# Optimization experiments

Hardware: AMD Instinct MI355X
Metric: run time of the kernel (lower is better)

## Reference

```python
import jax, jax.numpy as jnp
import numpy as np

STATE_DIM = 128
ACT_DIM = 32
ENC_K = 10   # encoder_spine_dim
DEC_K = 10   # decoder_dim
H0, H1 = 2048, 2048
BATCH = 16384
MAX_ACTION = 1.0
STD0 = 0.3872983346207417  # sqrt(0.15)


def setup_inputs() -> dict:
    key = jax.random.key(0)
    ks = jax.random.split(key, 10)
    state = jax.random.normal(ks[0], (BATCH, STATE_DIM), dtype=jnp.float32)
    # encoder params: mean linspace over mean_range, std constant
    mean_enc = jnp.broadcast_to(jnp.linspace(-3.0, 3.0, ENC_K, dtype=jnp.float32),
                                (1, STATE_DIM, ENC_K))
    std_enc = jnp.full((1, STATE_DIM, ENC_K), STD0, dtype=jnp.float32)
    def lin(k, fan_in, fan_out):
        bound = 1.0 / np.sqrt(fan_in)
        k1, k2 = jax.random.split(k)
        W = jax.random.uniform(k1, (fan_out, fan_in), jnp.float32, -bound, bound)
        b = jax.random.uniform(k2, (fan_out,), jnp.float32, -bound, bound)
        return W, b
    W1, b1 = lin(ks[1], STATE_DIM * ENC_K, H0)
    W2, b2 = lin(ks[2], H0, H1)
    W3, b3 = lin(ks[3], H1, ACT_DIM * DEC_K)
    # grouped conv1d: weight [act_dim, 1, dec_k], bias [act_dim]
    bound = 1.0 / np.sqrt(DEC_K)
    Wd = jax.random.uniform(ks[4], (ACT_DIM, 1, DEC_K), jnp.float32, -bound, bound)
    bd = jax.random.uniform(ks[5], (ACT_DIM,), jnp.float32, -bound, bound)
    return {"state": state, "mean_enc": mean_enc, "std_enc": std_enc,
            "W1": W1, "b1": b1, "W2": W2, "b2": b2, "W3": W3, "b3": b3,
            "Wd": Wd, "bd": bd}


def reference(state, mean_enc, std_enc, W1, b1, W2, b2, W3, b3, Wd, bd):
    # Population-coding encoder: sigmoid((obs - mean)/std), flattened
    spine = jax.nn.sigmoid((state[:, :, None] - mean_enc) / std_enc)  # [B, D, K]
    spine = spine.reshape(state.shape[0], -1)                         # [B, D*K]
    a = jax.nn.relu(spine @ W1.T + b1)
    a = jax.nn.relu(a @ W2.T + b2)
    a = a @ W3.T + b3                                                 # [B, A*Kd]
    d = a.reshape(-1, ACT_DIM, DEC_K)                                 # [B, A, Kd]
    # grouped Conv1d with kernel == length => per-channel dot product
    raw = jnp.einsum('bak,ak->ba', d, Wd[:, 0, :]) + bd               # [B, A]
    return MAX_ACTION * jnp.tanh(raw)
```

## Files before the change

### kernel.cpp

```cpp
#include <hip/hip_runtime.h>
#include <hip/hip_bf16.h>
#include <stdint.h>

#define BATCH   16384
#define SDIM    128
#define ENCK    10
#define ADIM    32
#define DECK    10
#define HID     2048
#define KSPINE  1280

typedef __bf16 bf16x8 __attribute__((ext_vector_type(8)));
typedef float  f32x4  __attribute__((ext_vector_type(4)));

typedef __attribute__((address_space(1))) const void kGlobalVoid;
typedef __attribute__((address_space(3))) void       kLdsVoid;

__device__ __forceinline__ unsigned short f2b(float f) {
  union { float f; unsigned u; } v; v.f = f;
  unsigned r = v.u + 0x7fffu + ((v.u >> 16) & 1u);
  return (unsigned short)(r >> 16);
}

__global__ void f2b_kernel(const float* __restrict__ in, unsigned* __restrict__ out, int n2) {
  int i = blockIdx.x * blockDim.x + threadIdx.x;
  if (i >= n2) return;
  float2 v = reinterpret_cast<const float2*>(in)[i];
  out[i] = (unsigned)f2b(v.x) | ((unsigned)f2b(v.y) << 16);
}

__global__ void encoder_kernel(const float* __restrict__ state,
                               const float* __restrict__ mean,
                               const float* __restrict__ stdv,
                               unsigned* __restrict__ spine) {
  int idx = blockIdx.x * blockDim.x + threadIdx.x;
  if (idx >= BATCH * SDIM) return;
  int d = idx & (SDIM - 1);
  float x = state[idx];
  float vals[ENCK];
#pragma unroll
  for (int k = 0; k < ENCK; ++k) {
    float z = (x - mean[d * ENCK + k]) / stdv[d * ENCK + k];
    vals[k] = 1.f / (1.f + __expf(-z));
  }
  unsigned* dst = spine + idx * (ENCK / 2);
#pragma unroll
  for (int k = 0; k < ENCK / 2; ++k)
    dst[k] = (unsigned)f2b(vals[2 * k]) | ((unsigned)f2b(vals[2 * k + 1]) << 16);
}

__global__ void weff_kernel(const float* __restrict__ W3, const float* __restrict__ Wd,
                            unsigned short* __restrict__ Weff) {
  int idx = blockIdx.x * 256 + threadIdx.x;
  int a = idx >> 11, j = idx & 2047;
  float s = 0.f;
#pragma unroll
  for (int k = 0; k < DECK; ++k)
    s += Wd[a * DECK + k] * W3[(size_t)(a * DECK + k) * HID + j];
  Weff[idx] = f2b(s);
}

__global__ void beff_kernel(const float* __restrict__ b3, const float* __restrict__ Wd,
                            const float* __restrict__ bd, float* __restrict__ beff) {
  int a = threadIdx.x;
  if (a >= ADIM) return;
  float s = bd[a];
#pragma unroll
  for (int k = 0; k < DECK; ++k) s += Wd[a * DECK + k] * b3[a * DECK + k];
  beff[a] = s;
}


#define A0B 0
#define B0B 32768
#define A1B 65536
#define B1B 98304

#define FENCE asm volatile("" ::: "memory")

#define STAGE(BASEPTR, R0A, R0B, LDS0, LDS1, KT)                                             \
  __builtin_amdgcn_global_load_lds((kGlobalVoid*)((BASEPTR) + (size_t)((R0A) + rs) * K + (KT) + ce), \
                                   (kLdsVoid*)(smem + (LDS0) + t * 16), 16, 0, 0);           \
  __builtin_amdgcn_global_load_lds((kGlobalVoid*)((BASEPTR) + (size_t)((R0B) + rs) * K + (KT) + ce), \
                                   (kLdsVoid*)(smem + (LDS1) + t * 16), 16, 0, 0);

#define PHASE(mp, ABASE, DOB, BBASE, DOVM, STAGES)                                           \
  do {                                                                                       \
    bf16x8 af[2][2];                                                                         \
    _Pragma("unroll")                                                                        \
    for (int j = 0; j < 2; ++j) {                                                            \
      _Pragma("unroll")                                                                      \
      for (int ks = 0; ks < 2; ++ks) {                                                       \
        int rowl = wr * 128 + ((mp) * 2 + j) * 16 + lr;                                      \
        af[j][ks] = *reinterpret_cast<const bf16x8*>(                                        \
            smem + (ABASE) + rowl * 128 + ((((ks) << 6) | (kh << 4)) ^ swz));                \
      }                                                                                      \
    }                                                                                        \
    if (DOB) {                                                                               \
      _Pragma("unroll")                                                                      \
      for (int n = 0; n < 4; ++n) {                                                          \
        _Pragma("unroll")                                                                    \
        for (int ks = 0; ks < 2; ++ks) {                                                     \
          int rowl = wc * 64 + n * 16 + lr;                                                  \
          bfv[n][ks] = *reinterpret_cast<const bf16x8*>(                                     \
              smem + (BBASE) + rowl * 128 + ((((ks) << 6) | (kh << 4)) ^ swz));              \
        }                                                                                    \
      }                                                                                      \
    }                                                                                        \
    STAGES                                                                                   \
    FENCE;                                                                                   \
    __builtin_amdgcn_s_barrier();                                                            \
    asm volatile("s_waitcnt lgkmcnt(0)" ::: "memory");                                       \
    __builtin_amdgcn_sched_barrier(0);                                                       \
    __builtin_amdgcn_s_setprio(1);                                                           \
    _Pragma("unroll")                                                                        \
    for (int j = 0; j < 2; ++j)                                                              \
      _Pragma("unroll")                                                                      \
      for (int n = 0; n < 4; ++n)                                                            \
        _Pragma("unroll")                                                                    \
        for (int ks = 0; ks < 2; ++ks)                                                       \
          acc[(mp) * 2 + j][n] =                                                             \
              __builtin_amdgcn_mfma_f32_16x16x32_bf16(af[j][ks], bfv[n][ks],                 \
                                                      acc[(mp) * 2 + j][n], 0, 0, 0);        \
    __builtin_amdgcn_s_setprio(0);                                                           \
    if (DOVM) asm volatile("s_waitcnt vmcnt(6)" ::: "memory");                               \
    FENCE;                                                                                   \
    __builtin_amdgcn_s_barrier();                                                            \
  } while (0)

__global__ __launch_bounds__(512, 2) void gemm256(
    const unsigned short* __restrict__ A,
    const unsigned short* __restrict__ Bw,
    const float* __restrict__ bias,
    unsigned short* __restrict__ Cout,
    int K, int NI) {
  __shared__ char smem[131072];

  const int t    = threadIdx.x;
  const int lane = t & 63;
  const int w    = t >> 6;
  const int wr   = w >> 2;
  const int wc   = w & 3;
  const int lr   = lane & 15;
  const int kh   = lane >> 4;
  const int swz  = (lr & 7) << 4;
  const int rs   = t >> 3;
  const int ce   = ((t & 7) ^ (rs & 7)) << 3;

  const int bid = blockIdx.x;
  const int xcd = bid & 7, idx = bid >> 3;
  const int row0 = (xcd * 8 + (idx >> 3)) * 256;
  const int col0 = (idx & 7) * 256;

  f32x4 acc[8][4];
#pragma unroll
  for (int m = 0; m < 8; ++m)
#pragma unroll
    for (int n = 0; n < 4; ++n)
      acc[m][n] = (f32x4){0.f, 0.f, 0.f, 0.f};

  bf16x8 bfv[4][2];

  STAGE(Bw, col0 + 0,   col0 + 64,  B0B + 0,     B0B + 8192,  0);
  STAGE(Bw, col0 + 128, col0 + 192, B0B + 16384, B0B + 24576, 0);
  STAGE(A,  row0 + 0,   row0 + 128, A0B + 0,     A0B + 16384, 0);
  STAGE(A,  row0 + 64,  row0 + 192, A0B + 8192,  A0B + 24576, 0);
  STAGE(Bw, col0 + 0,   col0 + 64,  B1B + 0,     B1B + 8192,  64);
  STAGE(Bw, col0 + 128, col0 + 192, B1B + 16384, B1B + 24576, 64);
  STAGE(A,  row0 + 0,   row0 + 128, A1B + 0,     A1B + 16384, 64);
  asm volatile("s_waitcnt vmcnt(6)" ::: "memory");
  FENCE;
  __builtin_amdgcn_s_barrier();

  for (int i = 0; i < NI; ++i) {
    int kt0 = i << 7;
    int kt1 = kt0 + 64;
    int kt2 = kt0 + 128; if (kt2 >= K) kt2 -= K;
    int kt3 = kt0 + 192; if (kt3 >= K) kt3 -= K;

    PHASE(0, A0B, true,  B0B, false, STAGE(A,  row0 + 64,  row0 + 192, A1B + 8192,  A1B + 24576, kt1));
    PHASE(1, A0B, false, B0B, false, STAGE(Bw, col0 + 0,   col0 + 64,  B0B + 0,     B0B + 8192,  kt2));
    PHASE(2, A0B, false, B0B, false, STAGE(Bw, col0 + 128, col0 + 192, B0B + 16384, B0B + 24576, kt2));
    PHASE(3, A0B, false, B0B, true,  STAGE(A,  row0 + 0,   row0 + 128, A0B + 0,     A0B + 16384, kt2));
    PHASE(0, A1B, true,  B1B, false, STAGE(A,  row0 + 64,  row0 + 192, A0B + 8192,  A0B + 24576, kt2));
    PHASE(1, A1B, false, B1B, false, STAGE(Bw, col0 + 0,   col0 + 64,  B1B + 0,     B1B + 8192,  kt3));
    PHASE(2, A1B, false, B1B, false, STAGE(Bw, col0 + 128, col0 + 192, B1B + 16384, B1B + 24576, kt3));
    PHASE(3, A1B, false, B1B, true,  STAGE(A,  row0 + 0,   row0 + 128, A1B + 0,     A1B + 16384, kt3));
  }

#pragma unroll
  for (int m = 0; m < 8; ++m) {
    int gr0 = row0 + wr * 128 + m * 16 + kh * 4;
#pragma unroll
    for (int n = 0; n < 4; ++n) {
      int gc = col0 + wc * 64 + n * 16 + lr;
      float bv = bias[gc];
#pragma unroll
      for (int v = 0; v < 4; ++v) {
        float val = fmaxf(acc[m][n][v] + bv, 0.f);
        Cout[(size_t)(gr0 + v) * 2048 + gc] = f2b(val);
      }
    }
  }
}

__global__ __launch_bounds__(128) void gemm_skinny(
    const unsigned short* __restrict__ A,
    const unsigned short* __restrict__ Bw,
    const float* __restrict__ beff,
    float* __restrict__ out) {
  const int t = threadIdx.x, lane = t & 63, w = t >> 6;
  const int lr = lane & 15, kh = lane >> 4;
  const int row0 = blockIdx.x * 64 + w * 32;
  f32x4 acc[2][2];
#pragma unroll
  for (int m = 0; m < 2; ++m)
#pragma unroll
    for (int n = 0; n < 2; ++n) acc[m][n] = (f32x4){0.f, 0.f, 0.f, 0.f};

#pragma unroll 4
  for (int kt = 0; kt < HID; kt += 32) {
    bf16x8 af[2], bv[2];
#pragma unroll
    for (int m = 0; m < 2; ++m)
      af[m] = *reinterpret_cast<const bf16x8*>(A + (size_t)(row0 + m * 16 + lr) * HID + kt + kh * 8);
#pragma unroll
    for (int n = 0; n < 2; ++n)
      bv[n] = *reinterpret_cast<const bf16x8*>(Bw + (size_t)(n * 16 + lr) * HID + kt + kh * 8);
#pragma unroll
    for (int m = 0; m < 2; ++m)
#pragma unroll
      for (int n = 0; n < 2; ++n)
        acc[m][n] = __builtin_amdgcn_mfma_f32_16x16x32_bf16(af[m], bv[n], acc[m][n], 0, 0, 0);
  }
#pragma unroll
  for (int m = 0; m < 2; ++m)
#pragma unroll
    for (int n = 0; n < 2; ++n)
#pragma unroll
      for (int v = 0; v < 4; ++v) {
        int row = row0 + m * 16 + kh * 4 + v;
        int col = n * 16 + lr;
        out[(size_t)row * ADIM + col] = tanhf(acc[m][n][v] + beff[col]);
      }
}

extern "C" void kernel_launch(void* const* d_in, const int* in_sizes, int n_in,
                              void* d_out, int out_size, void* d_ws, size_t ws_size,
                              hipStream_t stream) {
  const float* state    = (const float*)d_in[0];
  const float* mean_enc = (const float*)d_in[1];
  const float* std_enc  = (const float*)d_in[2];
  const float* W1 = (const float*)d_in[3];
  const float* b1 = (const float*)d_in[4];
  const float* W2 = (const float*)d_in[5];
  const float* b2 = (const float*)d_in[6];
  const float* W3 = (const float*)d_in[7];
  const float* b3 = (const float*)d_in[8];
  const float* Wd = (const float*)d_in[9];
  const float* bd = (const float*)d_in[10];

  char* ws = (char*)d_ws;
  unsigned short* W1b   = (unsigned short*)(ws + 0);
  unsigned short* W2b   = (unsigned short*)(ws + 5242880);
  unsigned short* Weff  = (unsigned short*)(ws + 13631488);
  float*          beff  = (float*)(ws + 13762560);
  unsigned short* spine = (unsigned short*)(ws + 13762688);
  unsigned short* h1    = (unsigned short*)(ws + 55705728);
  unsigned short* h2    = (unsigned short*)(ws + 122814592);

  f2b_kernel<<<5120, 256, 0, stream>>>(W1, (unsigned*)W1b, 1310720);
  f2b_kernel<<<8192, 256, 0, stream>>>(W2, (unsigned*)W2b, 2097152);
  weff_kernel<<<256, 256, 0, stream>>>(W3, Wd, Weff);
  beff_kernel<<<1, 64, 0, stream>>>(b3, Wd, bd, beff);

  encoder_kernel<<<(BATCH * SDIM) / 256, 256, 0, stream>>>(state, mean_enc, std_enc, (unsigned*)spine);

  gemm256<<<512, 512, 0, stream>>>(spine, W1b, b1, h1, KSPINE, KSPINE / 128);
  gemm256<<<512, 512, 0, stream>>>(h1,    W2b, b2, h2, HID,    HID / 128);
  gemm_skinny<<<BATCH / 64, 128, 0, stream>>>(h2, Weff, beff, (float*)d_out);
}
```

Measured before the change: 257.0 us.

## Software-pipeline LDS fragment loads in gemm256 and shrink skinny GEMM tiles

The main GEMM loop now double-buffers its register fragments. The next phase's A/B fragments are read from LDS right after the current MFMAs, and those MFMAs use fragments loaded in the previous phase, so LDS read latency overlaps with compute instead of sitting before each MFMA batch. The vmcnt wait moves to the start of a phase, and one barrier per phase is dropped. Separately, the skinny final GEMM gives each wave 16 rows instead of 32 and launches twice as many blocks, trading A-fragment reuse for more parallelism. The double buffers raise register pressure, and the barrier change alters synchronization around the LDS buffers.

```diff
diff --git a/kernel.cpp b/kernel.cpp
--- a/kernel.cpp
+++ b/kernel.cpp
@@ -84,46 +84,52 @@
   __builtin_amdgcn_global_load_lds((kGlobalVoid*)((BASEPTR) + (size_t)((R0B) + rs) * K + (KT) + ce), \
                                    (kLdsVoid*)(smem + (LDS1) + t * 16), 16, 0, 0);
 
-#define PHASE(mp, ABASE, DOB, BBASE, DOVM, STAGES)                                           \
+#define DS_AF(DST, ABASE, MPN)                                                               \
+  _Pragma("unroll")                                                                          \
+  for (int j2 = 0; j2 < 2; ++j2) {                                                           \
+    _Pragma("unroll")                                                                        \
+    for (int ks = 0; ks < 2; ++ks) {                                                         \
+      int rowl = wr * 128 + (MPN) * 32 + j2 * 16 + lr;                                       \
+      DST[j2][ks] = *reinterpret_cast<const bf16x8*>(                                        \
+          smem + (ABASE) + rowl * 128 + ((((ks) << 6) | (kh << 4)) ^ swz));                  \
+    }                                                                                        \
+  }
+
+#define DS_BF(DST, BBASE)                                                                    \
+  _Pragma("unroll")                                                                          \
+  for (int n = 0; n < 4; ++n) {                                                              \
+    _Pragma("unroll")                                                                        \
+    for (int ks = 0; ks < 2; ++ks) {                                                         \
+      int rowl = wc * 64 + n * 16 + lr;                                                      \
+      DST[n][ks] = *reinterpret_cast<const bf16x8*>(                                         \
+          smem + (BBASE) + rowl * 128 + ((((ks) << 6) | (kh << 4)) ^ swz));                  \
+    }                                                                                        \
+  }
+
+#define MFMA16(MP, AF, BF)                                                                   \
+  _Pragma("unroll")                                                                          \
+  for (int j2 = 0; j2 < 2; ++j2)                                                             \
+    _Pragma("unroll")                                                                        \
+    for (int n = 0; n < 4; ++n)                                                              \
+      _Pragma("unroll")                                                                      \
+      for (int ks = 0; ks < 2; ++ks)                                                         \
+        acc[(MP) * 2 + j2][n] = __builtin_amdgcn_mfma_f32_16x16x32_bf16(                     \
+            AF[j2][ks], BF[n][ks], acc[(MP) * 2 + j2][n], 0, 0, 0);
+
+#define PH(MP, AF_CUR, AF_NXT, BF_CUR, NXT_ABASE, NXT_MP, DOVM, DOB, NXT_BF, NXT_BBASE, STG) \
   do {                                                                                       \
-    bf16x8 af[2][2];                                                                         \
-    _Pragma("unroll")                                                                        \
-    for (int j = 0; j < 2; ++j) {                                                            \
-      _Pragma("unroll")                                                                      \
-      for (int ks = 0; ks < 2; ++ks) {                                                       \
-        int rowl = wr * 128 + ((mp) * 2 + j) * 16 + lr;                                      \
-        af[j][ks] = *reinterpret_cast<const bf16x8*>(                                        \
-            smem + (ABASE) + rowl * 128 + ((((ks) << 6) | (kh << 4)) ^ swz));                \
-      }                                                                                      \
-    }                                                                                        \
-    if (DOB) {                                                                               \
-      _Pragma("unroll")                                                                      \
-      for (int n = 0; n < 4; ++n) {                                                          \
-        _Pragma("unroll")                                                                    \
-        for (int ks = 0; ks < 2; ++ks) {                                                     \
-          int rowl = wc * 64 + n * 16 + lr;                                                  \
-          bfv[n][ks] = *reinterpret_cast<const bf16x8*>(                                     \
-              smem + (BBASE) + rowl * 128 + ((((ks) << 6) | (kh << 4)) ^ swz));              \
-        }                                                                                    \
-      }                                                                                      \
-    }                                                                                        \
-    STAGES                                                                                   \
-    FENCE;                                                                                   \
-    __builtin_amdgcn_s_barrier();                                                            \
     asm volatile("s_waitcnt lgkmcnt(0)" ::: "memory");                                       \
     __builtin_amdgcn_sched_barrier(0);                                                       \
+    if (DOVM) {                                                                              \
+      asm volatile("s_waitcnt vmcnt(6)" ::: "memory");                                       \
+      __builtin_amdgcn_sched_barrier(0);                                                     \
+    }                                                                                        \
     __builtin_amdgcn_s_setprio(1);                                                           \
-    _Pragma("unroll")                                                                        \
-    for (int j = 0; j < 2; ++j)                                                              \
-      _Pragma("unroll")                                                                      \
-      for (int n = 0; n < 4; ++n)                                                            \
-        _Pragma("unroll")                                                                    \
-        for (int ks = 0; ks < 2; ++ks)                                                       \
-          acc[(mp) * 2 + j][n] =                                                             \
-              __builtin_amdgcn_mfma_f32_16x16x32_bf16(af[j][ks], bfv[n][ks],                 \
-                                                      acc[(mp) * 2 + j][n], 0, 0, 0);        \
+    MFMA16(MP, AF_CUR, BF_CUR);                                                              \
     __builtin_amdgcn_s_setprio(0);                                                           \
-    if (DOVM) asm volatile("s_waitcnt vmcnt(6)" ::: "memory");                               \
+    DS_AF(AF_NXT, NXT_ABASE, NXT_MP);                                                        \
+    if (DOB) { DS_BF(NXT_BF, NXT_BBASE); }                                                   \
+    STG;                                                                                     \
     FENCE;                                                                                   \
     __builtin_amdgcn_s_barrier();                                                            \
   } while (0)
@@ -159,7 +165,7 @@
     for (int n = 0; n < 4; ++n)
       acc[m][n] = (f32x4){0.f, 0.f, 0.f, 0.f};
 
-  bf16x8 bfv[4][2];
+  bf16x8 af0[2][2], af1[2][2], bfv0[4][2], bfv1[4][2];
 
   STAGE(Bw, col0 + 0,   col0 + 64,  B0B + 0,     B0B + 8192,  0);
   STAGE(Bw, col0 + 128, col0 + 192, B0B + 16384, B0B + 24576, 0);
@@ -171,6 +177,8 @@
   asm volatile("s_waitcnt vmcnt(6)" ::: "memory");
   FENCE;
   __builtin_amdgcn_s_barrier();
+  DS_AF(af0, A0B, 0);
+  DS_BF(bfv0, B0B);
 
   for (int i = 0; i < NI; ++i) {
     int kt0 = i << 7;
@@ -178,14 +186,22 @@
     int kt2 = kt0 + 128; if (kt2 >= K) kt2 -= K;
     int kt3 = kt0 + 192; if (kt3 >= K) kt3 -= K;
 
-    PHASE(0, A0B, true,  B0B, false, STAGE(A,  row0 + 64,  row0 + 192, A1B + 8192,  A1B + 24576, kt1));
-    PHASE(1, A0B, false, B0B, false, STAGE(Bw, col0 + 0,   col0 + 64,  B0B + 0,     B0B + 8192,  kt2));
-    PHASE(2, A0B, false, B0B, false, STAGE(Bw, col0 + 128, col0 + 192, B0B + 16384, B0B + 24576, kt2));
-    PHASE(3, A0B, false, B0B, true,  STAGE(A,  row0 + 0,   row0 + 128, A0B + 0,     A0B + 16384, kt2));
-    PHASE(0, A1B, true,  B1B, false, STAGE(A,  row0 + 64,  row0 + 192, A0B + 8192,  A0B + 24576, kt2));
-    PHASE(1, A1B, false, B1B, false, STAGE(Bw, col0 + 0,   col0 + 64,  B1B + 0,     B1B + 8192,  kt3));
-    PHASE(2, A1B, false, B1B, false, STAGE(Bw, col0 + 128, col0 + 192, B1B + 16384, B1B + 24576, kt3));
-    PHASE(3, A1B, false, B1B, true,  STAGE(A,  row0 + 0,   row0 + 128, A1B + 0,     A1B + 16384, kt3));
+    PH(0, af0, af1, bfv0, A0B, 1, false, false, bfv1, B1B,
+       STAGE(A,  row0 + 64,  row0 + 192, A1B + 8192,  A1B + 24576, kt1));
+    PH(1, af1, af0, bfv0, A0B, 2, false, false, bfv1, B1B,
+       STAGE(Bw, col0 + 0,   col0 + 64,  B0B + 0,     B0B + 8192,  kt2));
+    PH(2, af0, af1, bfv0, A0B, 3, false, false, bfv1, B1B,
+       STAGE(Bw, col0 + 128, col0 + 192, B0B + 16384, B0B + 24576, kt2));
+    PH(3, af1, af0, bfv0, A1B, 0, true,  true,  bfv1, B1B,
+       STAGE(A,  row0 + 0,   row0 + 128, A0B + 0,     A0B + 16384, kt2));
+    PH(0, af0, af1, bfv1, A1B, 1, false, false, bfv0, B0B,
+       STAGE(A,  row0 + 64,  row0 + 192, A0B + 8192,  A0B + 24576, kt2));
+    PH(1, af1, af0, bfv1, A1B, 2, false, false, bfv0, B0B,
+       STAGE(Bw, col0 + 0,   col0 + 64,  B1B + 0,     B1B + 8192,  kt3));
+    PH(2, af0, af1, bfv1, A1B, 3, false, false, bfv0, B0B,
+       STAGE(Bw, col0 + 128, col0 + 192, B1B + 16384, B1B + 24576, kt3));
+    PH(3, af1, af0, bfv1, A0B, 0, true,  true,  bfv0, B0B,
+       STAGE(A,  row0 + 0,   row0 + 128, A1B + 0,     A1B + 16384, kt3));
   }
 
 #pragma unroll
@@ -211,38 +227,31 @@
     float* __restrict__ out) {
   const int t = threadIdx.x, lane = t & 63, w = t >> 6;
   const int lr = lane & 15, kh = lane >> 4;
-  const int row0 = blockIdx.x * 64 + w * 32;
-  f32x4 acc[2][2];
-#pragma unroll
-  for (int m = 0; m < 2; ++m)
-#pragma unroll
-    for (int n = 0; n < 2; ++n) acc[m][n] = (f32x4){0.f, 0.f, 0.f, 0.f};
+  const int row0 = (blockIdx.x * 2 + w) * 16;
+  f32x4 acc[2];
+  acc[0] = (f32x4){0.f, 0.f, 0.f, 0.f};
+  acc[1] = (f32x4){0.f, 0.f, 0.f, 0.f};
+
+  const unsigned short* Arow = A  + (size_t)(row0 + lr) * HID + kh * 8;
+  const unsigned short* B0   = Bw + (size_t)(lr) * HID + kh * 8;
+  const unsigned short* B1   = Bw + (size_t)(16 + lr) * HID + kh * 8;
 
 #pragma unroll 4
   for (int kt = 0; kt < HID; kt += 32) {
-    bf16x8 af[2], bv[2];
-#pragma unroll
-    for (int m = 0; m < 2; ++m)
-      af[m] = *reinterpret_cast<const bf16x8*>(A + (size_t)(row0 + m * 16 + lr) * HID + kt + kh * 8);
-#pragma unroll
-    for (int n = 0; n < 2; ++n)
-      bv[n] = *reinterpret_cast<const bf16x8*>(Bw + (size_t)(n * 16 + lr) * HID + kt + kh * 8);
-#pragma unroll
-    for (int m = 0; m < 2; ++m)
-#pragma unroll
-      for (int n = 0; n < 2; ++n)
-        acc[m][n] = __builtin_amdgcn_mfma_f32_16x16x32_bf16(af[m], bv[n], acc[m][n], 0, 0, 0);
-  }
-#pragma unroll
-  for (int m = 0; m < 2; ++m)
-#pragma unroll
-    for (int n = 0; n < 2; ++n)
-#pragma unroll
-      for (int v = 0; v < 4; ++v) {
-        int row = row0 + m * 16 + kh * 4 + v;
-        int col = n * 16 + lr;
-        out[(size_t)row * ADIM + col] = tanhf(acc[m][n][v] + beff[col]);
-      }
+    bf16x8 a  = *reinterpret_cast<const bf16x8*>(Arow + kt);
+    bf16x8 b0 = *reinterpret_cast<const bf16x8*>(B0 + kt);
+    bf16x8 b1 = *reinterpret_cast<const bf16x8*>(B1 + kt);
+    acc[0] = __builtin_amdgcn_mfma_f32_16x16x32_bf16(a, b0, acc[0], 0, 0, 0);
+    acc[1] = __builtin_amdgcn_mfma_f32_16x16x32_bf16(a, b1, acc[1], 0, 0, 0);
+  }
+#pragma unroll
+  for (int n = 0; n < 2; ++n)
+#pragma unroll
+    for (int v = 0; v < 4; ++v) {
+      int row = row0 + kh * 4 + v;
+      int col = n * 16 + lr;
+      out[(size_t)row * ADIM + col] = tanhf(acc[n][v] + beff[col]);
+    }
 }
 
 extern "C" void kernel_launch(void* const* d_in, const int* in_sizes, int n_in,
@@ -278,5 +287,5 @@
 
   gemm256<<<512, 512, 0, stream>>>(spine, W1b, b1, h1, KSPINE, KSPINE / 128);
   gemm256<<<512, 512, 0, stream>>>(h1,    W2b, b2, h2, HID,    HID / 128);
-  gemm_skinny<<<BATCH / 64, 128, 0, stream>>>(h2, Weff, beff, (float*)d_out);
-}
+  gemm_skinny<<<BATCH / 32, 128, 0, stream>>>(h2, Weff, beff, (float*)d_out);
+}
```

New measurement: 249.3 us. -3.0%, faster.
